# Optimization experiments

Measured on AMD Instinct MI355X. Metric: run time of the kernel, lower is better.

The kernel has to match this reference:

```python
import jax, jax.numpy as jnp
import numpy as np

BN_EPS = 1e-5


def setup_inputs() -> dict:
    key = jax.random.key(0)
    ks = jax.random.split(key, 5)
    b, c, h, w = 4, 128, 64, 64
    x = jax.random.normal(ks[0], (b, c, h, w), dtype=jnp.float32)
    # conv1x1 c -> 2c (fan-in scaled)
    w_inp = jax.random.normal(ks[1], (2 * c, c), dtype=jnp.float32) / np.sqrt(c)
    b_inp = jax.random.normal(ks[2], (2 * c,), dtype=jnp.float32) * 0.01
    bn_gamma = jnp.ones((2 * c,), dtype=jnp.float32)
    bn_beta = jnp.zeros((2 * c,), dtype=jnp.float32)
    bn_mean = jnp.zeros((2 * c,), dtype=jnp.float32)
    bn_var = jnp.ones((2 * c,), dtype=jnp.float32)
    w_out = jax.random.normal(ks[3], (c, c), dtype=jnp.float32) / np.sqrt(c)
    b_out = jax.random.normal(ks[4], (c,), dtype=jnp.float32) * 0.01
    return {
        "x": x, "w_inp": w_inp, "b_inp": b_inp,
        "bn_gamma": bn_gamma, "bn_beta": bn_beta,
        "bn_mean": bn_mean, "bn_var": bn_var,
        "w_out": w_out, "b_out": b_out,
    }


def reference(x, w_inp, b_inp, bn_gamma, bn_beta, bn_mean, bn_var, w_out, b_out):
    b, c, h, w = x.shape
    scale = c ** (-0.5)
    # project_inp: conv1x1 (c -> 2c) + BatchNorm2d (eval mode, running stats)
    t = jnp.einsum('bchw,oc->bohw', x, w_inp) + b_inp[None, :, None, None]
    bn_scale = bn_gamma * jax.lax.rsqrt(bn_var + BN_EPS)
    t = t * bn_scale[None, :, None, None] + (bn_beta - bn_mean * bn_scale)[None, :, None, None]
    # split qv along channels, flatten spatial to tokens: [b, N, c], N = h*w
    q = t[:, :c].reshape(b, c, h * w).transpose(0, 2, 1)
    v = t[:, c:].reshape(b, c, h * w).transpose(0, 2, 1)
    # self-similarity attention on q: [b, N, N]
    atn = jax.nn.softmax(jnp.einsum('bnc,bmc->bnm', q, q) * scale, axis=-1)
    y = jnp.einsum('bnm,bmc->bnc', atn, v)  # [b, N, c]
    y = y.transpose(0, 2, 1).reshape(b, c, h, w)
    # project_out: conv1x1 c -> c
    y = jnp.einsum('bchw,oc->bohw', y, w_out) + b_out[None, :, None, None]
    return (y, atn)
```

## Files before the change

### kernel.cpp

```cpp
#include <hip/hip_runtime.h>
#include <stdint.h>
#include <math.h>

#define C_DIM 128
#define N_TOK 4096
#define NB 4
#define LOG2E 1.4426950408889634f

typedef __attribute__((ext_vector_type(8))) short bf16x8;
typedef __attribute__((ext_vector_type(4))) short bf16x4;
typedef __attribute__((ext_vector_type(4))) float f32x4;

__device__ __forceinline__ unsigned short f2bf(float f) {
  unsigned u = __builtin_bit_cast(unsigned, f);
  unsigned r = (u + 0x7FFFu + ((u >> 16) & 1u)) >> 16;
  return (unsigned short)r;
}
__device__ __forceinline__ float bf2f(unsigned short h) {
  return __builtin_bit_cast(float, ((unsigned)h) << 16);
}
__device__ __forceinline__ void gload_lds16(const void* g, void* l) {
  __builtin_amdgcn_global_load_lds((const __attribute__((address_space(1))) void*)g,
                                   (__attribute__((address_space(3))) void*)l,
                                   16, 0, 0);
}

__global__ __launch_bounds__(256) void proj_in_kernel(
    const float* __restrict__ x, const float* __restrict__ w_inp,
    const float* __restrict__ b_inp, const float* __restrict__ gamma,
    const float* __restrict__ beta, const float* __restrict__ mean,
    const float* __restrict__ var,
    unsigned short* __restrict__ q, unsigned short* __restrict__ vT,
    int* __restrict__ m2bits) {
  __shared__ char smem[36096];
  unsigned short* xh = (unsigned short*)smem;
  unsigned short* xl = (unsigned short*)(smem + 17408);
  float* blkred = (float*)(smem + 35840);

  const int tid = threadIdx.x;
  const int b = blockIdx.x >> 6;
  const int n0 = (blockIdx.x & 63) << 6;
  const int lane = tid & 63;
  const int wave = tid >> 6;
  const int l15 = lane & 15, lg = lane >> 4;

  {
    const int c = tid >> 1;
    const int j0 = (tid & 1) * 32;
    const float* src = x + ((size_t)b * C_DIM + c) * N_TOK + n0 + j0;
#pragma unroll
    for (int j = 0; j < 32; j += 4) {
      float4 v4 = *(const float4*)(src + j);
#pragma unroll
      for (int e = 0; e < 4; e++) {
        float f = (&v4.x)[e];
        unsigned short hi = f2bf(f);
        unsigned short lo = f2bf(f - bf2f(hi));
        int n = j0 + j + e;
        xh[n * 136 + c] = hi;
        xl[n * 136 + c] = lo;
      }
    }
  }
  __syncthreads();

  f32x4 acc[4][4];
#pragma unroll
  for (int i = 0; i < 4; i++)
#pragma unroll
    for (int j = 0; j < 4; j++) acc[i][j] = {0.f, 0.f, 0.f, 0.f};

#pragma unroll
  for (int ks = 0; ks < 4; ks++) {
    bf16x8 ah[4], al[4];
#pragma unroll
    for (int ot = 0; ot < 4; ot++) {
      const int o = wave * 64 + ot * 16 + l15;
      const float* wp = w_inp + o * C_DIM + ks * 32 + lg * 8;
      float4 w0 = *(const float4*)wp;
      float4 w1 = *(const float4*)(wp + 4);
#pragma unroll
      for (int e = 0; e < 8; e++) {
        float f = (e < 4) ? (&w0.x)[e] : (&w1.x)[e - 4];
        unsigned short hi = f2bf(f);
        ah[ot][e] = (short)hi;
        al[ot][e] = (short)f2bf(f - bf2f(hi));
      }
    }
#pragma unroll
    for (int nt = 0; nt < 4; nt++) {
      const int off = (nt * 16 + l15) * 136 + ks * 32 + lg * 8;
      bf16x8 bh = *(const bf16x8*)(xh + off);
      bf16x8 bl = *(const bf16x8*)(xl + off);
#pragma unroll
      for (int ot = 0; ot < 4; ot++) {
        acc[ot][nt] = __builtin_amdgcn_mfma_f32_16x16x32_bf16(ah[ot], bh, acc[ot][nt], 0, 0, 0);
        acc[ot][nt] = __builtin_amdgcn_mfma_f32_16x16x32_bf16(ah[ot], bl, acc[ot][nt], 0, 0, 0);
        acc[ot][nt] = __builtin_amdgcn_mfma_f32_16x16x32_bf16(al[ot], bh, acc[ot][nt], 0, 0, 0);
      }
    }
  }
  __syncthreads();

  unsigned short* qT = (unsigned short*)smem;
  unsigned short* vTl = (unsigned short*)(smem + 17408);

#pragma unroll
  for (int ot = 0; ot < 4; ot++) {
#pragma unroll
    for (int r = 0; r < 4; r++) {
      const int o = wave * 64 + ot * 16 + lg * 4 + r;
      float A = gamma[o] * rsqrtf(var[o] + 1e-5f);
      float Bo = beta[o] + (b_inp[o] - mean[o]) * A;
#pragma unroll
      for (int nt = 0; nt < 4; nt++) {
        float val = acc[ot][nt][r] * A + Bo;
        unsigned short hv = f2bf(val);
        int n = nt * 16 + l15;
        if (wave < 2) {
          qT[n * 136 + o] = hv;
        } else {
          vTl[(o - 128) * 72 + n] = hv;
        }
      }
    }
  }
  __syncthreads();
  {
    int j = tid >> 2, c0 = (tid & 3) * 32;
    unsigned short* dst = q + ((size_t)b * N_TOK + n0 + j) * C_DIM + c0;
    const unsigned short* s = qT + j * 136 + c0;
#pragma unroll
    for (int i = 0; i < 32; i += 8) *(bf16x8*)(dst + i) = *(const bf16x8*)(s + i);
  }
  {
    int c = tid >> 1, h = (tid & 1) * 32;
    unsigned short* dst = vT + ((size_t)b * C_DIM + c) * N_TOK + n0 + h;
    const unsigned short* s = vTl + c * 72 + h;
#pragma unroll
    for (int i = 0; i < 32; i += 8) *(bf16x8*)(dst + i) = *(const bf16x8*)(s + i);
  }
  {
    int row = tid >> 2, qn = tid & 3;
    const unsigned short* qr = qT + row * 136 + qn * 32;
    float s = 0.f;
#pragma unroll
    for (int i = 0; i < 32; i++) {
      float f = bf2f(qr[i]);
      s = fmaf(f, f, s);
    }
    s += __shfl_xor(s, 1);
    s += __shfl_xor(s, 2);
    if ((tid & 3) == 0) blkred[row] = s;
    __syncthreads();
    if (tid < 64) {
      float v = blkred[tid];
      v = fmaxf(v, __shfl_xor(v, 1));
      v = fmaxf(v, __shfl_xor(v, 2));
      v = fmaxf(v, __shfl_xor(v, 4));
      v = fmaxf(v, __shfl_xor(v, 8));
      v = fmaxf(v, __shfl_xor(v, 16));
      v = fmaxf(v, __shfl_xor(v, 32));
      if (tid == 0) atomicMax(m2bits, __float_as_int(v));
    }
  }
}

__global__ __launch_bounds__(256, 4) void attn_kernel(
    const unsigned short* __restrict__ q, const unsigned short* __restrict__ vT,
    const float* __restrict__ w_out, const float* __restrict__ b_out,
    float* __restrict__ yout, float* __restrict__ atn,
    const float* __restrict__ m2ptr) {
  __shared__ char smem[37888];

  const int tid = threadIdx.x;
  const int lane = tid & 63;
  const int kq = tid >> 6;
  const int l15 = lane & 15, lg = lane >> 4, l7 = lane & 7;
  const int bid = (int)((blockIdx.x & 7) * 128 + (blockIdx.x >> 3));
  const int b = bid >> 8;
  const int row0 = (bid & 255) << 4;

  const unsigned short* qb = q + (size_t)b * N_TOK * C_DIM;
  const unsigned short* vb = vT + (size_t)b * C_DIM * N_TOK;

  const float scale = 0.08838834764831845f;
  const float ke = scale * LOG2E;
  const float nmk = -(m2ptr[0]) * ke;

  bf16x8 qf[4];
#pragma unroll
  for (int ks = 0; ks < 4; ks++)
    qf[ks] = *(const bf16x8*)(qb + (size_t)(row0 + l15) * C_DIM + ks * 32 + lg * 8);

  int koff[4];
#pragma unroll
  for (int ks = 0; ks < 4; ks++) koff[ks] = (ks * 64 + lg * 16) ^ (l7 * 16);
  const int kqbase = kq * 4096 + l15 * 256;

  auto stageK = [&](int kt, int buf) {
    char* base = smem + buf * 16384;
#pragma unroll
    for (int i = 0; i < 4; i++) {
      int lin = i * 256 + tid;
      int key = lin >> 4;
      int c = ((lin & 15) * 8) ^ ((key & 7) * 8);
      gload_lds16(qb + (size_t)(kt * 64 + key) * C_DIM + c, base + lin * 16);
    }
  };

  unsigned short* pbw = (unsigned short*)(smem + 32768) + l15 * 72 + kq * 16 + lg * 4;
  const char* parb = smem + 32768 + l15 * 144;
  float* statsL = (float*)(smem + 37376);

  const unsigned short* vl0 = vb + (size_t)((kq * 2 + 0) * 16 + l15) * N_TOK + lg * 8;
  const unsigned short* vl1 = vb + (size_t)((kq * 2 + 1) * 16 + l15) * N_TOK + lg * 8;

  float lpart = 0.f;
  f32x4 yacc[2];
  yacc[0] = {0.f, 0.f, 0.f, 0.f};
  yacc[1] = {0.f, 0.f, 0.f, 0.f};

  bf16x8 vA[2][2], vB[2][2];
  stageK(0, 0);
#pragma unroll
  for (int ks2 = 0; ks2 < 2; ks2++) {
    vA[0][ks2] = *(const bf16x8*)(vl0 + ks2 * 32);
    vA[1][ks2] = *(const bf16x8*)(vl1 + ks2 * 32);
  }
  __syncthreads();

  auto sweep1_iter = [&](int kt, bf16x8(&vc)[2][2], bf16x8(&vn)[2][2]) {
    const char* kb = smem + (kt & 1) * 16384;
    f32x4 acc = {0.f, 0.f, 0.f, 0.f};
#pragma unroll
    for (int ks = 0; ks < 4; ks++) {
      bf16x8 ak = *(const bf16x8*)(kb + kqbase + koff[ks]);
      acc = __builtin_amdgcn_mfma_f32_16x16x32_bf16(ak, qf[ks], acc, 0, 0, 0);
    }
    bf16x4 pk;
#pragma unroll
    for (int r = 0; r < 4; r++) {
      float p = __builtin_amdgcn_exp2f(fmaf(acc[r], ke, nmk));
      lpart += p;
      pk[r] = (short)f2bf(p);
    }
    *(bf16x4*)(pbw + (kt & 1) * 1152) = pk;
    if (kt + 1 < 64) stageK(kt + 1, (kt + 1) & 1);
    __syncthreads();
    const char* pbt = parb + (kt & 1) * 2304;
#pragma unroll
    for (int ks2 = 0; ks2 < 2; ks2++) {
      bf16x8 ap = *(const bf16x8*)(pbt + ks2 * 64 + lg * 16);
      yacc[0] = __builtin_amdgcn_mfma_f32_16x16x32_bf16(ap, vc[0][ks2], yacc[0], 0, 0, 0);
      yacc[1] = __builtin_amdgcn_mfma_f32_16x16x32_bf16(ap, vc[1][ks2], yacc[1], 0, 0, 0);
    }
    if (kt + 1 < 64) {
      const unsigned short* v0 = vl0 + (size_t)(kt + 1) * 64;
      const unsigned short* v1 = vl1 + (size_t)(kt + 1) * 64;
#pragma unroll
      for (int ks2 = 0; ks2 < 2; ks2++) {
        vn[0][ks2] = *(const bf16x8*)(v0 + ks2 * 32);
        vn[1][ks2] = *(const bf16x8*)(v1 + ks2 * 32);
      }
    }
  };

  for (int kt = 0; kt < 64; kt += 2) {
    sweep1_iter(kt, vA, vB);
    sweep1_iter(kt + 1, vB, vA);
  }

  lpart += __shfl_xor(lpart, 16);
  lpart += __shfl_xor(lpart, 32);
  if (lg == 0) statsL[kq * 16 + l15] = lpart;
  __syncthreads();

  float invl_r[4];
#pragma unroll
  for (int r = 0; r < 4; r++) {
    const int row = lg * 4 + r;
    invl_r[r] = 1.0f / (statsL[row] + statsL[16 + row] + statsL[32 + row] + statsL[48 + row]);
  }
  const float invl2 =
      1.0f / (statsL[l15] + statsL[16 + l15] + statsL[32 + l15] + statsL[48 + l15]);

  __syncthreads();
  {
    unsigned short* yl = (unsigned short*)smem;
    float* ol = (float*)(smem + 8192);
#pragma unroll
    for (int ctl = 0; ctl < 2; ctl++)
#pragma unroll
      for (int r = 0; r < 4; r++)
        yl[(lg * 4 + r) * 136 + (kq * 2 + ctl) * 16 + l15] = f2bf(yacc[ctl][r] * invl_r[r]);
    __syncthreads();

    bf16x8 af[4];
#pragma unroll
    for (int ks = 0; ks < 4; ks++)
      af[ks] = *(const bf16x8*)(yl + l15 * 136 + ks * 32 + lg * 8);

#pragma unroll
    for (int cotl = 0; cotl < 2; cotl++) {
      const int cot = kq * 2 + cotl;
      f32x4 oacc = {0.f, 0.f, 0.f, 0.f};
#pragma unroll
      for (int ks = 0; ks < 4; ks++) {
        const float* wp = w_out + (cot * 16 + l15) * C_DIM + ks * 32 + lg * 8;
        float4 w0 = *(const float4*)wp;
        float4 w1 = *(const float4*)(wp + 4);
        bf16x8 bw;
#pragma unroll
        for (int e = 0; e < 8; e++) bw[e] = (short)f2bf((e < 4) ? (&w0.x)[e] : (&w1.x)[e - 4]);
        oacc = __builtin_amdgcn_mfma_f32_16x16x32_bf16(af[ks], bw, oacc, 0, 0, 0);
      }
      float bo = b_out[cot * 16 + l15];
#pragma unroll
      for (int r = 0; r < 4; r++) ol[(cot * 16 + l15) * 20 + lg * 4 + r] = oacc[r] + bo;
    }
    __syncthreads();
    {
      const int co = tid >> 1;
      const int r0 = (tid & 1) * 8;
      float* dst = yout + ((size_t)b * C_DIM + co) * N_TOK + row0 + r0;
      const float* s = ol + co * 20 + r0;
      *(float4*)dst = *(const float4*)s;
      *(float4*)(dst + 4) = *(const float4*)(s + 4);
    }
  }
  __syncthreads();

  stageK(0, 0);
  __syncthreads();
  float* atnp = atn + ((size_t)b * N_TOK + row0 + l15) * N_TOK + kq * 16 + lg * 4;
  for (int kt = 0; kt < 64; kt++) {
    const char* kb = smem + (kt & 1) * 16384;
    f32x4 acc = {0.f, 0.f, 0.f, 0.f};
#pragma unroll
    for (int ks = 0; ks < 4; ks++) {
      bf16x8 ak = *(const bf16x8*)(kb + kqbase + koff[ks]);
      acc = __builtin_amdgcn_mfma_f32_16x16x32_bf16(ak, qf[ks], acc, 0, 0, 0);
    }
    f32x4 o;
#pragma unroll
    for (int r = 0; r < 4; r++)
      o[r] = __builtin_amdgcn_exp2f(fmaf(acc[r], ke, nmk)) * invl2;
    __builtin_nontemporal_store(o, (f32x4*)(atnp + (size_t)kt * 64));
    if (kt + 1 < 64) stageK(kt + 1, (kt + 1) & 1);
    __syncthreads();
  }
}

extern "C" void kernel_launch(void* const* d_in, const int* in_sizes, int n_in,
                              void* d_out, int out_size, void* d_ws, size_t ws_size,
                              hipStream_t stream) {
  const float* x = (const float*)d_in[0];
  const float* w_inp = (const float*)d_in[1];
  const float* b_inp = (const float*)d_in[2];
  const float* gamma = (const float*)d_in[3];
  const float* beta = (const float*)d_in[4];
  const float* mean = (const float*)d_in[5];
  const float* var = (const float*)d_in[6];
  const float* w_out = (const float*)d_in[7];
  const float* b_out = (const float*)d_in[8];

  float* out = (float*)d_out;
  float* yout = out;
  float* atn = out + (size_t)NB * C_DIM * N_TOK;

  unsigned short* q = (unsigned short*)d_ws;
  unsigned short* vT = q + (size_t)NB * N_TOK * C_DIM;
  int* m2bits = (int*)(vT + (size_t)NB * C_DIM * N_TOK);

  hipMemsetAsync(m2bits, 0, 4, stream);
  proj_in_kernel<<<256, 256, 0, stream>>>(x, w_inp, b_inp, gamma, beta, mean, var, q, vT, m2bits);
  attn_kernel<<<1024, 256, 0, stream>>>(q, vT, w_out, b_out, yout, atn, (const float*)m2bits);
}
```

Measured before the change: 250.6 us.

## Issue K/V prefetch earlier and replace syncthreads with explicit vmcnt waits

```diff
diff --git a/kernel.cpp b/kernel.cpp
--- a/kernel.cpp
+++ b/kernel.cpp
@@ -10,6 +10,11 @@
 typedef __attribute__((ext_vector_type(8))) short bf16x8;
 typedef __attribute__((ext_vector_type(4))) short bf16x4;
 typedef __attribute__((ext_vector_type(4))) float f32x4;
+
+#define WAIT_VM(N) asm volatile("s_waitcnt vmcnt(" #N ")" ::: "memory")
+#define WAIT_LGKM0 asm volatile("s_waitcnt lgkmcnt(0)" ::: "memory")
+#define SBAR() __builtin_amdgcn_s_barrier()
+#define SCHED_FENCE() __builtin_amdgcn_sched_barrier(0)
 
 __device__ __forceinline__ unsigned short f2bf(float f) {
   unsigned u = __builtin_bit_cast(unsigned, f);
@@ -228,9 +233,26 @@
     vA[0][ks2] = *(const bf16x8*)(vl0 + ks2 * 32);
     vA[1][ks2] = *(const bf16x8*)(vl1 + ks2 * 32);
   }
-  __syncthreads();
+  WAIT_VM(0);
+  SBAR();
+  SCHED_FENCE();
 
   auto sweep1_iter = [&](int kt, bf16x8(&vc)[2][2], bf16x8(&vn)[2][2]) {
+    if (kt + 1 < 64) {
+      stageK(kt + 1, (kt + 1) & 1);
+      const unsigned short* v0 = vl0 + (size_t)(kt + 1) * 64;
+      const unsigned short* v1 = vl1 + (size_t)(kt + 1) * 64;
+#pragma unroll
+      for (int ks2 = 0; ks2 < 2; ks2++) {
+        vn[0][ks2] = *(const bf16x8*)(v0 + ks2 * 32);
+        vn[1][ks2] = *(const bf16x8*)(v1 + ks2 * 32);
+      }
+      WAIT_VM(8);
+    } else {
+      WAIT_VM(0);
+    }
+    SBAR();
+    SCHED_FENCE();
     const char* kb = smem + (kt & 1) * 16384;
     f32x4 acc = {0.f, 0.f, 0.f, 0.f};
 #pragma unroll
@@ -246,23 +268,15 @@
       pk[r] = (short)f2bf(p);
     }
     *(bf16x4*)(pbw + (kt & 1) * 1152) = pk;
-    if (kt + 1 < 64) stageK(kt + 1, (kt + 1) & 1);
-    __syncthreads();
+    WAIT_LGKM0;
+    SBAR();
+    SCHED_FENCE();
     const char* pbt = parb + (kt & 1) * 2304;
 #pragma unroll
     for (int ks2 = 0; ks2 < 2; ks2++) {
       bf16x8 ap = *(const bf16x8*)(pbt + ks2 * 64 + lg * 16);
       yacc[0] = __builtin_amdgcn_mfma_f32_16x16x32_bf16(ap, vc[0][ks2], yacc[0], 0, 0, 0);
       yacc[1] = __builtin_amdgcn_mfma_f32_16x16x32_bf16(ap, vc[1][ks2], yacc[1], 0, 0, 0);
-    }
-    if (kt + 1 < 64) {
-      const unsigned short* v0 = vl0 + (size_t)(kt + 1) * 64;
-      const unsigned short* v1 = vl1 + (size_t)(kt + 1) * 64;
-#pragma unroll
-      for (int ks2 = 0; ks2 < 2; ks2++) {
-        vn[0][ks2] = *(const bf16x8*)(v0 + ks2 * 32);
-        vn[1][ks2] = *(const bf16x8*)(v1 + ks2 * 32);
-      }
     }
   };
 
@@ -332,9 +346,19 @@
   __syncthreads();
 
   stageK(0, 0);
-  __syncthreads();
+  WAIT_VM(0);
+  SBAR();
+  SCHED_FENCE();
   float* atnp = atn + ((size_t)b * N_TOK + row0 + l15) * N_TOK + kq * 16 + lg * 4;
   for (int kt = 0; kt < 64; kt++) {
+    if (kt + 1 < 64) {
+      stageK(kt + 1, (kt + 1) & 1);
+      WAIT_VM(5);
+    } else {
+      WAIT_VM(1);
+    }
+    SBAR();
+    SCHED_FENCE();
     const char* kb = smem + (kt & 1) * 16384;
     f32x4 acc = {0.f, 0.f, 0.f, 0.f};
 #pragma unroll
@@ -346,9 +370,9 @@
 #pragma unroll
     for (int r = 0; r < 4; r++)
       o[r] = __builtin_amdgcn_exp2f(fmaf(acc[r], ke, nmk)) * invl2;
-    __builtin_nontemporal_store(o, (f32x4*)(atnp + (size_t)kt * 64));
-    if (kt + 1 < 64) stageK(kt + 1, (kt + 1) & 1);
-    __syncthreads();
+    *(f32x4*)(atnp + (size_t)kt * 64) = o;
+    SBAR();
+    SCHED_FENCE();
   }
 }
 
```

Measured after the change: 241.1 us. 3.8% less time.
